# Performance work log

Hardware: AMD Instinct MI355X
Metric: run time of the kernel (lower is better)

The kernel has to match this reference:

```python
import math
import jax, jax.numpy as jnp
import numpy as np

N, E = 20000, 640000
S_DIM, Z_DIM, H, QK, VD = 64, 64, 4, 8, 8
EPS = 1e-8


def quat_rotate(v, q):
    # v: [..., 3], q: [..., 4] (w, x, y, z), broadcastable. Unit-quaternion rotation:
    # v' = v + 2*(w*(u x v) + u x (u x v))
    w = q[..., 0:1]
    u = q[..., 1:4]
    uv = jnp.cross(u, v)
    return v + 2.0 * (w * uv + jnp.cross(u, uv))


def setup_inputs() -> dict:
    key = jax.random.key(0)
    ks = jax.random.split(key, 16)
    s = jax.random.normal(ks[0], (N, S_DIM), dtype=jnp.float32)
    z = jax.random.normal(ks[1], (E, Z_DIM), dtype=jnp.float32)
    edge_index = jax.random.randint(ks[2], (2, E), 0, N)
    quaternion = jax.random.normal(ks[3], (N, 4), dtype=jnp.float32)
    quaternion = quaternion / jnp.linalg.norm(quaternion, axis=-1, keepdims=True)
    translation = jax.random.normal(ks[4], (N, 3), dtype=jnp.float32)
    sc_s = 1.0 / math.sqrt(S_DIM)
    sc_z = 1.0 / math.sqrt(Z_DIM)
    # weights stored [in, out] so y = x @ W (equivalent to torch x @ W.T)
    Wq_s = jax.random.normal(ks[5], (S_DIM, H * S_DIM), dtype=jnp.float32) * sc_s
    Wk_s = jax.random.normal(ks[6], (S_DIM, H * S_DIM), dtype=jnp.float32) * sc_s
    Wv_s = jax.random.normal(ks[7], (S_DIM, H * S_DIM), dtype=jnp.float32) * sc_s
    Wq_v = jax.random.normal(ks[8], (S_DIM, H * QK * 3), dtype=jnp.float32) * sc_s
    Wk_v = jax.random.normal(ks[9], (S_DIM, H * QK * 3), dtype=jnp.float32) * sc_s
    Wv_v = jax.random.normal(ks[10], (S_DIM, H * VD * 3), dtype=jnp.float32) * sc_s
    Wb = jax.random.normal(ks[11], (Z_DIM, H), dtype=jnp.float32) * sc_z
    bb = jnp.zeros((H,), dtype=jnp.float32)
    Wdz = jax.random.normal(ks[12], (Z_DIM, Z_DIM // 4), dtype=jnp.float32) * sc_z
    bdz = jnp.zeros((Z_DIM // 4,), dtype=jnp.float32)
    head_weights = jnp.full((H,), 0.541324854612918, dtype=jnp.float32)  # softplus^{-1}(1)
    concat_dim = Z_DIM // 4 + S_DIM + VD * 4
    Wout = jax.random.normal(ks[13], (H * concat_dim, S_DIM), dtype=jnp.float32) / math.sqrt(H * concat_dim)
    bout = jnp.zeros((S_DIM,), dtype=jnp.float32)
    return {
        's': s, 'z': z, 'edge_index': edge_index, 'quaternion': quaternion,
        'translation': translation, 'Wq_s': Wq_s, 'Wk_s': Wk_s, 'Wv_s': Wv_s,
        'Wq_v': Wq_v, 'Wk_v': Wk_v, 'Wv_v': Wv_v, 'Wb': Wb, 'bb': bb,
        'Wdz': Wdz, 'bdz': bdz, 'head_weights': head_weights,
        'Wout': Wout, 'bout': bout,
    }


def reference(s, z, edge_index, quaternion, translation,
              Wq_s, Wk_s, Wv_s, Wq_v, Wk_v, Wv_v,
              Wb, bb, Wdz, bdz, head_weights, Wout, bout):
    idx_i, idx_j = edge_index[0], edge_index[1]
    n = s.shape[0]
    h = head_weights.shape[0]
    qk = Wq_v.shape[1] // (3 * h)
    vd = Wv_v.shape[1] // (3 * h)

    q_scalar = (s @ Wq_s).reshape(n, h, -1)
    k_scalar = (s @ Wk_s).reshape(n, h, -1)
    v_scalar = (s @ Wv_s).reshape(n, h, -1)

    def to_points(x):
        # torch.split into 3 chunks then stack(dim=-1): [n, 3*c] -> [n, c, 3]
        c = x.shape[-1] // 3
        return jnp.swapaxes(x.reshape(n, 3, c), 1, 2)

    quat_b = quaternion[:, None, :]
    trans_b = translation[:, None, :]
    q_vec = (quat_rotate(to_points(s @ Wq_v), quat_b) + trans_b).reshape(n, h, qk, 3)
    k_vec = (quat_rotate(to_points(s @ Wk_v), quat_b) + trans_b).reshape(n, h, qk, 3)
    v_vec = (quat_rotate(to_points(s @ Wv_v), quat_b) + trans_b).reshape(n, h, vd, 3)

    b_bias = z @ Wb + bb  # [E, H]

    attn = jnp.sum(k_scalar[idx_i] * q_scalar[idx_j], axis=-1)  # [E, H]
    attn = attn * math.sqrt(1.0 / 3 * qk) + math.sqrt(1.0 / 3) * b_bias

    disp = q_vec[idx_i] - k_vec[idx_j]            # [E, H, qk, 3]
    vec_att = jnp.sum(disp * disp, axis=-1)       # [E, H, qk]
    hw = jax.nn.softplus(head_weights)[None, :, None]
    vec_att = jnp.sum(vec_att * hw, axis=-1) * math.sqrt(1.0 / (3 * (qk * 9.0 / 2))) * (-0.5)
    attn = attn + vec_att

    # segment softmax over destination node idx_i
    seg_max = jax.ops.segment_max(attn, idx_i, num_segments=n)
    ea = jnp.exp(attn - seg_max[idx_i])
    denom = jax.ops.segment_sum(ea, idx_i, num_segments=n)
    attn = ea / denom[idx_i]                      # [E, H]

    out_scalar = jax.ops.segment_sum(attn[:, :, None] * v_scalar[idx_i], idx_i, num_segments=n)
    out_scalar = out_scalar.reshape(n, -1)

    out_vec = jax.ops.segment_sum(attn[:, :, None, None] * v_vec[idx_i], idx_i, num_segments=n)
    out_vec = out_vec - translation[:, None, None, :]
    q_conj = jnp.concatenate([quaternion[:, :1], -quaternion[:, 1:]], axis=-1)
    out_vec = quat_rotate(out_vec, q_conj[:, None, None, :])   # [n, h, vd, 3]
    out_vec_norm = jnp.sqrt(jnp.sum(out_vec * out_vec, axis=-1) + EPS).reshape(n, -1)
    out_vec_flat = out_vec.reshape(n, -1, 3)

    pair_z = z @ Wdz + bdz                         # [E, z/4]
    out_pair = jax.ops.segment_sum(attn[:, :, None] * pair_z[:, None, :], idx_i, num_segments=n)
    out_pair = out_pair.reshape(n, -1)

    feats = jnp.concatenate([out_scalar,
                             out_vec_flat[..., 0], out_vec_flat[..., 1], out_vec_flat[..., 2],
                             out_vec_norm, out_pair], axis=-1)
    return feats @ Wout + bout
```

## Files before the change

### kernel.cpp

```cpp
#include <hip/hip_runtime.h>
#include <stdint.h>


#define C_SQRT83  1.6329931618554518f
#define C_SQRT13  0.5773502691896258f
#define C_VEC    -0.04811252243246881f

__device__ __forceinline__ unsigned short f2bf(float f){
  unsigned u = __float_as_uint(f);
  u += 0x7fffu + ((u >> 16) & 1u);
  return (unsigned short)(u >> 16);
}
__device__ __forceinline__ unsigned pack2(float a, float b){
  return (unsigned)f2bf(a) | ((unsigned)f2bf(b) << 16);
}
__device__ __forceinline__ float bflo(unsigned u){ return __uint_as_float(u << 16); }
__device__ __forceinline__ float bfhi(unsigned u){ return __uint_as_float(u & 0xffff0000u); }

__device__ __forceinline__ void quat_rot(float w, float ux, float uy, float uz,
                                         float vx, float vy, float vz,
                                         float& ox, float& oy, float& oz){
  float cx = uy*vz - uz*vy;
  float cy = uz*vx - ux*vz;
  float cz = ux*vy - uy*vx;
  float dx = uy*cz - uz*cy;
  float dy = uz*cx - ux*cz;
  float dz = ux*cy - uy*cx;
  ox = vx + 2.f*(w*cx + dx);
  oy = vy + 2.f*(w*cy + dy);
  oz = vz + 2.f*(w*cz + dz);
}


__global__ __launch_bounds__(256) void k_count(const int* __restrict__ ei,
                                               unsigned* __restrict__ counts,
                                               unsigned* __restrict__ rank, int ne){
  int e = blockIdx.x*256 + threadIdx.x;
  if (e >= ne) return;
  rank[e] = atomicAdd(&counts[ei[e]], 1u);
}

__global__ __launch_bounds__(256) void k_scan(const unsigned* __restrict__ counts,
                                              unsigned* __restrict__ row_off, int n){
  __shared__ unsigned part[256];
  int t = threadIdx.x;
  int chunk = (n + 255) >> 8;
  int s0 = t*chunk, s1 = min(s0 + chunk, n);
  unsigned sum = 0;
  for (int k = s0; k < s1; ++k) sum += counts[k];
  part[t] = sum; __syncthreads();
  for (int off = 1; off < 256; off <<= 1){
    unsigned v = (t >= off) ? part[t-off] : 0u;
    __syncthreads();
    part[t] += v;
    __syncthreads();
  }
  unsigned run = (t == 0) ? 0u : part[t-1];
  for (int k = s0; k < s1; ++k){
    row_off[k] = run; run += counts[k];
  }
  if (t == 255) row_off[n] = part[255];
}

__global__ __launch_bounds__(256) void k_fill(const int* __restrict__ ei,
                                              const unsigned* __restrict__ rank,
                                              const unsigned* __restrict__ roff,
                                              unsigned* __restrict__ si,
                                              unsigned* __restrict__ sj,
                                              unsigned* __restrict__ se, int ne){
  int e = blockIdx.x*256 + threadIdx.x;
  if (e >= ne) return;
  const int i = ei[e];
  const unsigned pos = roff[i] + rank[e];
  si[pos] = (unsigned)i;
  sj[pos] = (unsigned)ei[ne + e];
  se[pos] = (unsigned)e;
}


#define BN 32

__device__ __forceinline__ void pass256(const float* __restrict__ W,
                                        const float stT[64][40], int cg, int sl,
                                        float acc[8][4]){
  #pragma unroll
  for (int i=0;i<8;i++){ acc[i][0]=0.f; acc[i][1]=0.f; acc[i][2]=0.f; acc[i][3]=0.f; }
  #pragma unroll 4
  for (int k = 0; k < 64; ++k){
    const float4 w  = *(const float4*)(W + (size_t)k*256 + cg*4);
    const float4 n0 = *(const float4*)&stT[k][sl*8];
    const float4 n1 = *(const float4*)&stT[k][sl*8+4];
    acc[0][0]+=n0.x*w.x; acc[0][1]+=n0.x*w.y; acc[0][2]+=n0.x*w.z; acc[0][3]+=n0.x*w.w;
    acc[1][0]+=n0.y*w.x; acc[1][1]+=n0.y*w.y; acc[1][2]+=n0.y*w.z; acc[1][3]+=n0.y*w.w;
    acc[2][0]+=n0.z*w.x; acc[2][1]+=n0.z*w.y; acc[2][2]+=n0.z*w.z; acc[2][3]+=n0.z*w.w;
    acc[3][0]+=n0.w*w.x; acc[3][1]+=n0.w*w.y; acc[3][2]+=n0.w*w.z; acc[3][3]+=n0.w*w.w;
    acc[4][0]+=n1.x*w.x; acc[4][1]+=n1.x*w.y; acc[4][2]+=n1.x*w.z; acc[4][3]+=n1.x*w.w;
    acc[5][0]+=n1.y*w.x; acc[5][1]+=n1.y*w.y; acc[5][2]+=n1.y*w.z; acc[5][3]+=n1.y*w.w;
    acc[6][0]+=n1.z*w.x; acc[6][1]+=n1.z*w.y; acc[6][2]+=n1.z*w.z; acc[6][3]+=n1.z*w.w;
    acc[7][0]+=n1.w*w.x; acc[7][1]+=n1.w*w.y; acc[7][2]+=n1.w*w.z; acc[7][3]+=n1.w*w.w;
  }
}

__device__ __forceinline__ void pass96(const float* __restrict__ W,
                                       const float stT[64][40], int cgp, int slp,
                                       float acc[4][4]){
  #pragma unroll
  for (int i=0;i<4;i++){ acc[i][0]=0.f; acc[i][1]=0.f; acc[i][2]=0.f; acc[i][3]=0.f; }
  if (cgp >= 24) return;
  #pragma unroll 4
  for (int k = 0; k < 64; ++k){
    const float4 w = *(const float4*)(W + (size_t)k*96 + cgp*4);
    const float4 nv = *(const float4*)&stT[k][slp*4];
    acc[0][0]+=nv.x*w.x; acc[0][1]+=nv.x*w.y; acc[0][2]+=nv.x*w.z; acc[0][3]+=nv.x*w.w;
    acc[1][0]+=nv.y*w.x; acc[1][1]+=nv.y*w.y; acc[1][2]+=nv.y*w.z; acc[1][3]+=nv.y*w.w;
    acc[2][0]+=nv.z*w.x; acc[2][1]+=nv.z*w.y; acc[2][2]+=nv.z*w.z; acc[2][3]+=nv.z*w.w;
    acc[3][0]+=nv.w*w.x; acc[3][1]+=nv.w*w.y; acc[3][2]+=nv.w*w.z; acc[3][3]+=nv.w*w.w;
  }
}

__global__ __launch_bounds__(256) void k_proj(
    const float* __restrict__ s, const float* __restrict__ quat, const float* __restrict__ trans,
    const float* __restrict__ Wqs, const float* __restrict__ Wks, const float* __restrict__ Wvs,
    const float* __restrict__ Wqv, const float* __restrict__ Wkv, const float* __restrict__ Wvv,
    unsigned* __restrict__ qs, unsigned* __restrict__ ks, float* __restrict__ vs,
    unsigned* __restrict__ qv, unsigned* __restrict__ kv, float* __restrict__ vv, int n)
{
  __shared__ float stT[64][40];
  __shared__ float pt[BN][97];
  const int tid = threadIdx.x;
  const int node0 = blockIdx.x * BN;

  #pragma unroll
  for (int r = 0; r < 2; ++r){
    const int idx = tid + r*256;
    const int nd = idx >> 4, c4 = idx & 15;
    const int g = node0 + nd;
    float4 v = make_float4(0.f,0.f,0.f,0.f);
    if (g < n) v = *(const float4*)(s + (size_t)g*64 + c4*4);
    stT[c4*4+0][nd]=v.x; stT[c4*4+1][nd]=v.y; stT[c4*4+2][nd]=v.z; stT[c4*4+3][nd]=v.w;
  }
  __syncthreads();

  const int cg = tid & 63, sl = tid >> 6;
  const int cgp = tid & 31, slp = tid >> 5;
  float acc[8][4];

  pass256(Wqs, stT, cg, sl, acc);
  #pragma unroll
  for (int i=0;i<8;i++){
    const int g = node0 + sl*8 + i;
    if (g < n){
      uint2 u; u.x = pack2(acc[i][0],acc[i][1]); u.y = pack2(acc[i][2],acc[i][3]);
      *(uint2*)(qs + (size_t)g*128 + cg*2) = u;
    }
  }
  pass256(Wks, stT, cg, sl, acc);
  #pragma unroll
  for (int i=0;i<8;i++){
    const int g = node0 + sl*8 + i;
    if (g < n){
      uint2 u; u.x = pack2(acc[i][0],acc[i][1]); u.y = pack2(acc[i][2],acc[i][3]);
      *(uint2*)(ks + (size_t)g*128 + cg*2) = u;
    }
  }
  pass256(Wvs, stT, cg, sl, acc);
  #pragma unroll
  for (int i=0;i<8;i++){
    const int g = node0 + sl*8 + i;
    if (g < n){
      float4 f; f.x=acc[i][0]; f.y=acc[i][1]; f.z=acc[i][2]; f.w=acc[i][3];
      *(float4*)(vs + (size_t)g*256 + cg*4) = f;
    }
  }

  float pac[4][4];

  pass96(Wqv, stT, cgp, slp, pac);
  __syncthreads();
  if (cgp < 24){
    #pragma unroll
    for (int i=0;i<4;i++){
      #pragma unroll
      for (int c=0;c<4;c++) pt[slp*4+i][cgp*4+c] = pac[i][c];
    }
  }
  __syncthreads();
  #pragma unroll
  for (int r = 0; r < 2; ++r){
    const int t2 = tid + r*256;
    const int nd = t2 >> 4, pp = t2 & 15;
    const int g = node0 + nd;
    if (g < n){
      const float4 q4 = *(const float4*)(quat + (size_t)g*4);
      const float tx = trans[(size_t)g*3], ty = trans[(size_t)g*3+1], tz = trans[(size_t)g*3+2];
      float x0,y0,z0,x1,y1,z1;
      quat_rot(q4.x,q4.y,q4.z,q4.w, pt[nd][2*pp],   pt[nd][32+2*pp],   pt[nd][64+2*pp],   x0,y0,z0);
      quat_rot(q4.x,q4.y,q4.z,q4.w, pt[nd][2*pp+1], pt[nd][32+2*pp+1], pt[nd][64+2*pp+1], x1,y1,z1);
      x0+=tx; y0+=ty; z0+=tz; x1+=tx; y1+=ty; z1+=tz;
      unsigned* d = qv + (size_t)g*48 + pp*3;
      d[0] = pack2(x0,y0); d[1] = pack2(z0,x1); d[2] = pack2(y1,z1);
    }
  }

  pass96(Wkv, stT, cgp, slp, pac);
  __syncthreads();
  if (cgp < 24){
    #pragma unroll
    for (int i=0;i<4;i++){
      #pragma unroll
      for (int c=0;c<4;c++) pt[slp*4+i][cgp*4+c] = pac[i][c];
    }
  }
  __syncthreads();
  #pragma unroll
  for (int r = 0; r < 2; ++r){
    const int t2 = tid + r*256;
    const int nd = t2 >> 4, pp = t2 & 15;
    const int g = node0 + nd;
    if (g < n){
      const float4 q4 = *(const float4*)(quat + (size_t)g*4);
      const float tx = trans[(size_t)g*3], ty = trans[(size_t)g*3+1], tz = trans[(size_t)g*3+2];
      float x0,y0,z0,x1,y1,z1;
      quat_rot(q4.x,q4.y,q4.z,q4.w, pt[nd][2*pp],   pt[nd][32+2*pp],   pt[nd][64+2*pp],   x0,y0,z0);
      quat_rot(q4.x,q4.y,q4.z,q4.w, pt[nd][2*pp+1], pt[nd][32+2*pp+1], pt[nd][64+2*pp+1], x1,y1,z1);
      x0+=tx; y0+=ty; z0+=tz; x1+=tx; y1+=ty; z1+=tz;
      unsigned* d = kv + (size_t)g*48 + pp*3;
      d[0] = pack2(x0,y0); d[1] = pack2(z0,x1); d[2] = pack2(y1,z1);
    }
  }

  pass96(Wvv, stT, cgp, slp, pac);
  __syncthreads();
  if (cgp < 24){
    #pragma unroll
    for (int i=0;i<4;i++){
      #pragma unroll
      for (int c=0;c<4;c++) pt[slp*4+i][cgp*4+c] = pac[i][c];
    }
  }
  __syncthreads();
  #pragma unroll
  for (int r = 0; r < 12; ++r){
    const int idx = tid + r*256;
    const int nd = idx / 96, col = idx - nd*96;
    const int g = node0 + nd;
    if (g < n) vv[(size_t)g*96 + col] = pt[nd][col];
  }
}


__global__ __launch_bounds__(256) void k_edge(
    const float* __restrict__ z,
    const unsigned* __restrict__ si, const unsigned* __restrict__ sj, const unsigned* __restrict__ se,
    const float* __restrict__ Wb,  const float* __restrict__ bb,
    const float* __restrict__ Wdz, const float* __restrict__ bdz,
    const float* __restrict__ hwts,
    const unsigned* __restrict__ qs, const unsigned* __restrict__ ks,
    const unsigned* __restrict__ qv, const unsigned* __restrict__ kv,
    float* __restrict__ logits, unsigned* __restrict__ pz, int ne)
{
  const int p = blockIdx.x*256 + threadIdx.x;
  if (p >= ne) return;
  const unsigned i = si[p], j = sj[p], e = se[p];

  float b4[4];  b4[0]=b4[1]=b4[2]=b4[3]=0.f;
  float pacc[16];
  #pragma unroll
  for (int c=0;c<16;c++) pacc[c]=0.f;
  const float* zr = z + (size_t)e*64;
  #pragma unroll
  for (int k4 = 0; k4 < 16; ++k4){
    const float4 zv = *(const float4*)(zr + 4*k4);
    #pragma unroll
    for (int kk = 0; kk < 4; ++kk){
      const int k = 4*k4 + kk;
      const float zk = (kk==0)?zv.x:((kk==1)?zv.y:((kk==2)?zv.z:zv.w));
      const float4 wb = *(const float4*)(Wb + k*4);
      b4[0]+=zk*wb.x; b4[1]+=zk*wb.y; b4[2]+=zk*wb.z; b4[3]+=zk*wb.w;
      const float* wd = Wdz + k*16;
      const float4 w0=*(const float4*)(wd), w1=*(const float4*)(wd+4),
                   w2=*(const float4*)(wd+8), w3=*(const float4*)(wd+12);
      pacc[ 0]+=zk*w0.x; pacc[ 1]+=zk*w0.y; pacc[ 2]+=zk*w0.z; pacc[ 3]+=zk*w0.w;
      pacc[ 4]+=zk*w1.x; pacc[ 5]+=zk*w1.y; pacc[ 6]+=zk*w1.z; pacc[ 7]+=zk*w1.w;
      pacc[ 8]+=zk*w2.x; pacc[ 9]+=zk*w2.y; pacc[10]+=zk*w2.z; pacc[11]+=zk*w2.w;
      pacc[12]+=zk*w3.x; pacc[13]+=zk*w3.y; pacc[14]+=zk*w3.z; pacc[15]+=zk*w3.w;
    }
  }
  #pragma unroll
  for (int c=0;c<16;c++) pacc[c] += bdz[c];
  { uint4 u0, u1;
    u0.x=pack2(pacc[0],pacc[1]);   u0.y=pack2(pacc[2],pacc[3]);
    u0.z=pack2(pacc[4],pacc[5]);   u0.w=pack2(pacc[6],pacc[7]);
    u1.x=pack2(pacc[8],pacc[9]);   u1.y=pack2(pacc[10],pacc[11]);
    u1.z=pack2(pacc[12],pacc[13]); u1.w=pack2(pacc[14],pacc[15]);
    uint4* d = (uint4*)(pz + (size_t)p*8);
    d[0]=u0; d[1]=u1; }

  const uint4* kr = (const uint4*)(ks + (size_t)i*128);
  const uint4* qr = (const uint4*)(qs + (size_t)j*128);
  float sdot[4];
  #pragma unroll
  for (int h = 0; h < 4; ++h){
    float acc = 0.f;
    #pragma unroll
    for (int c = 0; c < 8; ++c){
      const uint4 a = kr[h*8+c];
      const uint4 b = qr[h*8+c];
      acc += bflo(a.x)*bflo(b.x) + bfhi(a.x)*bfhi(b.x);
      acc += bflo(a.y)*bflo(b.y) + bfhi(a.y)*bfhi(b.y);
      acc += bflo(a.z)*bflo(b.z) + bfhi(a.z)*bfhi(b.z);
      acc += bflo(a.w)*bflo(b.w) + bfhi(a.w)*bfhi(b.w);
    }
    sdot[h] = acc;
  }

  const uint4* qvr = (const uint4*)(qv + (size_t)i*48);
  const uint4* kvr = (const uint4*)(kv + (size_t)j*48);
  float vsum[4];
  #pragma unroll
  for (int h = 0; h < 4; ++h){
    float acc = 0.f;
    #pragma unroll
    for (int c = 0; c < 3; ++c){
      const uint4 a = qvr[h*3+c];
      const uint4 b = kvr[h*3+c];
      float d;
      d = bflo(a.x)-bflo(b.x); acc += d*d;  d = bfhi(a.x)-bfhi(b.x); acc += d*d;
      d = bflo(a.y)-bflo(b.y); acc += d*d;  d = bfhi(a.y)-bfhi(b.y); acc += d*d;
      d = bflo(a.z)-bflo(b.z); acc += d*d;  d = bfhi(a.z)-bfhi(b.z); acc += d*d;
      d = bflo(a.w)-bflo(b.w); acc += d*d;  d = bfhi(a.w)-bfhi(b.w); acc += d*d;
    }
    vsum[h] = acc;
  }

  float4 lg;
  {
    float l[4];
    #pragma unroll
    for (int h = 0; h < 4; ++h){
      const float hw = log1pf(__expf(hwts[h]));
      l[h] = C_SQRT83*sdot[h] + C_SQRT13*(b4[h] + bb[h]) + C_VEC*hw*vsum[h];
    }
    lg.x=l[0]; lg.y=l[1]; lg.z=l[2]; lg.w=l[3];
  }
  *(float4*)(logits + (size_t)p*4) = lg;
}


__global__ __launch_bounds__(256) void k_soft(
    const float* __restrict__ logits, const unsigned* __restrict__ pz,
    const unsigned* __restrict__ row_off, float* __restrict__ out_pair, int n)
{
  const int node = blockIdx.x*4 + (threadIdx.x >> 6);
  if (node >= n) return;
  const int lane = threadIdx.x & 63;
  const int beg = (int)row_off[node], end = (int)row_off[node+1];

  float m[4] = {-3.0e38f,-3.0e38f,-3.0e38f,-3.0e38f};
  for (int p = beg + lane; p < end; p += 64){
    const float4 l = *(const float4*)(logits + (size_t)p*4);
    m[0]=fmaxf(m[0],l.x); m[1]=fmaxf(m[1],l.y); m[2]=fmaxf(m[2],l.z); m[3]=fmaxf(m[3],l.w);
  }
  #pragma unroll
  for (int msk = 1; msk < 64; msk <<= 1){
    #pragma unroll
    for (int h=0;h<4;h++) m[h] = fmaxf(m[h], __shfl_xor(m[h], msk));
  }
  float S[4] = {0.f,0.f,0.f,0.f};
  for (int p = beg + lane; p < end; p += 64){
    const float4 l = *(const float4*)(logits + (size_t)p*4);
    S[0]+=__expf(l.x-m[0]); S[1]+=__expf(l.y-m[1]);
    S[2]+=__expf(l.z-m[2]); S[3]+=__expf(l.w-m[3]);
  }
  #pragma unroll
  for (int msk = 1; msk < 64; msk <<= 1){
    #pragma unroll
    for (int h=0;h<4;h++) S[h] += __shfl_xor(S[h], msk);
  }
  float inv[4];
  #pragma unroll
  for (int h=0;h<4;h++) inv[h] = (S[h] > 0.f) ? (1.f/S[h]) : 0.f;

  const int e4 = lane >> 4, c = lane & 15;
  float acc[4] = {0.f,0.f,0.f,0.f};
  for (int base = beg; base < end; base += 4){
    const int p = base + e4;
    if (p < end){
      const float4 l = *(const float4*)(logits + (size_t)p*4);
      const unsigned u = pz[(size_t)p*8 + (c>>1)];
      const float pzv = (c & 1) ? bfhi(u) : bflo(u);
      acc[0] += __expf(l.x-m[0]) * pzv;
      acc[1] += __expf(l.y-m[1]) * pzv;
      acc[2] += __expf(l.z-m[2]) * pzv;
      acc[3] += __expf(l.w-m[3]) * pzv;
    }
  }
  #pragma unroll
  for (int msk = 16; msk < 64; msk <<= 1){
    #pragma unroll
    for (int h=0;h<4;h++) acc[h] += __shfl_xor(acc[h], msk);
  }
  const int hOut = lane >> 4;
  out_pair[(size_t)node*64 + lane] = acc[hOut] * inv[hOut];
}


__global__ __launch_bounds__(256) void k_out(
    const float* __restrict__ vs, const float* __restrict__ vv,
    const float* __restrict__ out_pair, const unsigned* __restrict__ row_off,
    const float* __restrict__ quat, const float* __restrict__ trans,
    const float* __restrict__ Wout, const float* __restrict__ bout,
    float* __restrict__ out, int n)
{
  __shared__ float feats[32][448];
  __shared__ int degs[32];
  const int tid = threadIdx.x;
  const int node0 = blockIdx.x*32;

  if (tid < 32){
    const int g = node0 + tid;
    degs[tid] = (g < n) ? (int)(row_off[g+1] - row_off[g]) : 1;
  }
  __syncthreads();

  for (int x = tid; x < 32*256; x += 256){
    const int nd = x >> 8, c = x & 255;
    const int g = node0 + nd;
    feats[nd][c] = (g < n && degs[nd] > 0) ? vs[(size_t)g*256 + c] : 0.f;
  }
  for (int x = tid; x < 32*64; x += 256){
    const int nd = x >> 6, c = x & 63;
    const int g = node0 + nd;
    feats[nd][384 + c] = (g < n) ? out_pair[(size_t)g*64 + c] : 0.f;
  }
  for (int x = tid; x < 32*32; x += 256){
    const int nd = x >> 5, pt = x & 31;
    const int g = node0 + nd;
    float X=0.f, Y=0.f, Z=0.f;
    if (g < n){
      if (degs[nd] > 0){
        X = vv[(size_t)g*96 + pt];
        Y = vv[(size_t)g*96 + 32 + pt];
        Z = vv[(size_t)g*96 + 64 + pt];
      } else {
        const float4 q4 = *(const float4*)(quat + (size_t)g*4);
        const float tx = trans[(size_t)g*3], ty = trans[(size_t)g*3+1], tz = trans[(size_t)g*3+2];
        quat_rot(q4.x, -q4.y, -q4.z, -q4.w, -tx, -ty, -tz, X, Y, Z);
      }
    }
    feats[nd][256 + pt] = X;
    feats[nd][288 + pt] = Y;
    feats[nd][320 + pt] = Z;
    feats[nd][352 + pt] = sqrtf(X*X + Y*Y + Z*Z + 1e-8f);
  }
  __syncthreads();

  const int lane = tid & 63;
  const int wave = tid >> 6;
  float acc[8];
  #pragma unroll
  for (int q8=0;q8<8;q8++) acc[q8]=0.f;

  for (int k0 = 0; k0 < 448; k0 += 4){
    const float w0 = Wout[(size_t)(k0+0)*64 + lane];
    const float w1 = Wout[(size_t)(k0+1)*64 + lane];
    const float w2 = Wout[(size_t)(k0+2)*64 + lane];
    const float w3 = Wout[(size_t)(k0+3)*64 + lane];
    #pragma unroll
    for (int q8 = 0; q8 < 8; ++q8){
      const float4 f = *(const float4*)&feats[wave*8 + q8][k0];
      acc[q8] += f.x*w0 + f.y*w1 + f.z*w2 + f.w*w3;
    }
  }
  const float bo = bout[lane];
  #pragma unroll
  for (int q8 = 0; q8 < 8; ++q8){
    const int g = node0 + wave*8 + q8;
    if (g < n) out[(size_t)g*64 + lane] = acc[q8] + bo;
  }
}


extern "C" void kernel_launch(void* const* d_in, const int* in_sizes, int n_in,
                              void* d_out, int out_size, void* d_ws, size_t ws_size,
                              hipStream_t stream) {
  const float* s     = (const float*)d_in[0];
  const float* z     = (const float*)d_in[1];
  const int*   ei    = (const int*)  d_in[2];
  const float* quat  = (const float*)d_in[3];
  const float* trans = (const float*)d_in[4];
  const float* Wqs   = (const float*)d_in[5];
  const float* Wks   = (const float*)d_in[6];
  const float* Wvs   = (const float*)d_in[7];
  const float* Wqv   = (const float*)d_in[8];
  const float* Wkv   = (const float*)d_in[9];
  const float* Wvv   = (const float*)d_in[10];
  const float* Wb    = (const float*)d_in[11];
  const float* bb    = (const float*)d_in[12];
  const float* Wdz   = (const float*)d_in[13];
  const float* bdz   = (const float*)d_in[14];
  const float* hwts  = (const float*)d_in[15];
  const float* Wout  = (const float*)d_in[16];
  const float* bout  = (const float*)d_in[17];
  float* out = (float*)d_out;

  const int n  = in_sizes[0] / 64;
  const int ne = in_sizes[1] / 64;

  size_t off = 0;
  char* base = (char*)d_ws;
  auto take = [&](size_t bytes)->char* {
    char* p = base + off;
    off += (bytes + 255) & ~(size_t)255;
    return p;
  };
  unsigned* qs     = (unsigned*)take((size_t)n*512);
  unsigned* ks     = (unsigned*)take((size_t)n*512);
  unsigned* qvt    = (unsigned*)take((size_t)n*192);
  unsigned* kvt    = (unsigned*)take((size_t)n*192);
  float*    vs     = (float*)   take((size_t)n*1024);
  float*    vv     = (float*)   take((size_t)n*384);
  float*    logits = (float*)   take((size_t)ne*16);
  unsigned* pz     = (unsigned*)take((size_t)ne*32);
  unsigned* counts = (unsigned*)take((size_t)n*4);
  unsigned* roff   = (unsigned*)take((size_t)(n+1)*4);
  unsigned* rank   = (unsigned*)take((size_t)ne*4);
  unsigned* si     = (unsigned*)take((size_t)ne*4);
  unsigned* sj     = (unsigned*)take((size_t)ne*4);
  unsigned* se     = (unsigned*)take((size_t)ne*4);
  float*    opair  = (float*)   take((size_t)n*256);
  (void)ws_size; (void)n_in; (void)out_size;

  const int gbE = (ne + 255) / 256;

  hipMemsetAsync(counts, 0, (size_t)n*4, stream);
  k_count<<<gbE, 256, 0, stream>>>(ei, counts, rank, ne);
  k_scan <<<1,   256, 0, stream>>>(counts, roff, n);
  k_fill <<<gbE, 256, 0, stream>>>(ei, rank, roff, si, sj, se, ne);
  k_proj <<<(n + BN - 1)/BN, 256, 0, stream>>>(s, quat, trans, Wqs, Wks, Wvs, Wqv, Wkv, Wvv,
                                               qs, ks, vs, qvt, kvt, vv, n);
  k_edge <<<gbE, 256, 0, stream>>>(z, si, sj, se, Wb, bb, Wdz, bdz, hwts,
                                   qs, ks, qvt, kvt, logits, pz, ne);
  k_soft <<<(n + 3)/4, 256, 0, stream>>>(logits, pz, roff, opair, n);
  k_out  <<<(n + 31)/32, 256, 0, stream>>>(vs, vv, opair, roff, quat, trans,
                                           Wout, bout, out, n);
}
```

Before: 659.8 us.

## Split z projection into coalesced edge-order kernel, gather by edge id later

Moves the z @ Wb and z @ Wdz projections out of the sorted-order edge kernel into a separate kernel that reads z in original edge order, so the 64-float rows are read coalesced instead of gathered through the permutation. The edge kernel now gathers only a 16-byte bias row per edge, and the softmax kernel gathers the packed pair projection through se. This adds a kernel launch and an extra intermediate write and read of the bias, and it turns the pair reads in k_soft into indirect gathers.

```diff
diff --git a/kernel.cpp b/kernel.cpp
--- a/kernel.cpp
+++ b/kernel.cpp
@@ -249,24 +249,20 @@
 }
 
 
-__global__ __launch_bounds__(256) void k_edge(
+__global__ __launch_bounds__(256) void k_zp(
     const float* __restrict__ z,
-    const unsigned* __restrict__ si, const unsigned* __restrict__ sj, const unsigned* __restrict__ se,
     const float* __restrict__ Wb,  const float* __restrict__ bb,
     const float* __restrict__ Wdz, const float* __restrict__ bdz,
-    const float* __restrict__ hwts,
-    const unsigned* __restrict__ qs, const unsigned* __restrict__ ks,
-    const unsigned* __restrict__ qv, const unsigned* __restrict__ kv,
-    float* __restrict__ logits, unsigned* __restrict__ pz, int ne)
+    float* __restrict__ zb, unsigned* __restrict__ zpz, int ne)
 {
-  const int p = blockIdx.x*256 + threadIdx.x;
-  if (p >= ne) return;
-  const unsigned i = si[p], j = sj[p], e = se[p];
-
-  float b4[4];  b4[0]=b4[1]=b4[2]=b4[3]=0.f;
-  float pacc[16];
-  #pragma unroll
-  for (int c=0;c<16;c++) pacc[c]=0.f;
+  const int e = blockIdx.x*256 + threadIdx.x;
+  if (e >= ne) return;
+
+  float b4[4]; float pacc[16];
+  b4[0]=bb[0]; b4[1]=bb[1]; b4[2]=bb[2]; b4[3]=bb[3];
+  #pragma unroll
+  for (int c=0;c<16;c++) pacc[c] = bdz[c];
+
   const float* zr = z + (size_t)e*64;
   #pragma unroll
   for (int k4 = 0; k4 < 16; ++k4){
@@ -286,15 +282,30 @@
       pacc[12]+=zk*w3.x; pacc[13]+=zk*w3.y; pacc[14]+=zk*w3.z; pacc[15]+=zk*w3.w;
     }
   }
-  #pragma unroll
-  for (int c=0;c<16;c++) pacc[c] += bdz[c];
+  *(float4*)(zb + (size_t)e*4) = make_float4(b4[0],b4[1],b4[2],b4[3]);
   { uint4 u0, u1;
     u0.x=pack2(pacc[0],pacc[1]);   u0.y=pack2(pacc[2],pacc[3]);
     u0.z=pack2(pacc[4],pacc[5]);   u0.w=pack2(pacc[6],pacc[7]);
     u1.x=pack2(pacc[8],pacc[9]);   u1.y=pack2(pacc[10],pacc[11]);
     u1.z=pack2(pacc[12],pacc[13]); u1.w=pack2(pacc[14],pacc[15]);
-    uint4* d = (uint4*)(pz + (size_t)p*8);
+    uint4* d = (uint4*)(zpz + (size_t)e*8);
     d[0]=u0; d[1]=u1; }
+}
+
+
+__global__ __launch_bounds__(256) void k_edge(
+    const float* __restrict__ zb,
+    const unsigned* __restrict__ si, const unsigned* __restrict__ sj, const unsigned* __restrict__ se,
+    const float* __restrict__ hwts,
+    const unsigned* __restrict__ qs, const unsigned* __restrict__ ks,
+    const unsigned* __restrict__ qv, const unsigned* __restrict__ kv,
+    float* __restrict__ logits, int ne)
+{
+  const int p = blockIdx.x*256 + threadIdx.x;
+  if (p >= ne) return;
+  const unsigned i = si[p], j = sj[p], e = se[p];
+
+  const float4 b4 = *(const float4*)(zb + (size_t)e*4);
 
   const uint4* kr = (const uint4*)(ks + (size_t)i*128);
   const uint4* qr = (const uint4*)(qs + (size_t)j*128);
@@ -333,13 +344,14 @@
     vsum[h] = acc;
   }
 
+  const float bias[4] = {b4.x, b4.y, b4.z, b4.w};
   float4 lg;
   {
     float l[4];
     #pragma unroll
     for (int h = 0; h < 4; ++h){
       const float hw = log1pf(__expf(hwts[h]));
-      l[h] = C_SQRT83*sdot[h] + C_SQRT13*(b4[h] + bb[h]) + C_VEC*hw*vsum[h];
+      l[h] = C_SQRT83*sdot[h] + C_SQRT13*bias[h] + C_VEC*hw*vsum[h];
     }
     lg.x=l[0]; lg.y=l[1]; lg.z=l[2]; lg.w=l[3];
   }
@@ -348,7 +360,8 @@
 
 
 __global__ __launch_bounds__(256) void k_soft(
-    const float* __restrict__ logits, const unsigned* __restrict__ pz,
+    const float* __restrict__ logits, const unsigned* __restrict__ zpz,
+    const unsigned* __restrict__ se,
     const unsigned* __restrict__ row_off, float* __restrict__ out_pair, int n)
 {
   const int node = blockIdx.x*4 + (threadIdx.x >> 6);
@@ -387,7 +400,8 @@
     const int p = base + e4;
     if (p < end){
       const float4 l = *(const float4*)(logits + (size_t)p*4);
-      const unsigned u = pz[(size_t)p*8 + (c>>1)];
+      const unsigned e = se[p];
+      const unsigned u = zpz[(size_t)e*8 + (c>>1)];
       const float pzv = (c & 1) ? bfhi(u) : bflo(u);
       acc[0] += __expf(l.x-m[0]) * pzv;
       acc[1] += __expf(l.y-m[1]) * pzv;
@@ -521,7 +535,8 @@
   float*    vs     = (float*)   take((size_t)n*1024);
   float*    vv     = (float*)   take((size_t)n*384);
   float*    logits = (float*)   take((size_t)ne*16);
-  unsigned* pz     = (unsigned*)take((size_t)ne*32);
+  float*    zb     = (float*)   take((size_t)ne*16);
+  unsigned* zpz    = (unsigned*)take((size_t)ne*32);
   unsigned* counts = (unsigned*)take((size_t)n*4);
   unsigned* roff   = (unsigned*)take((size_t)(n+1)*4);
   unsigned* rank   = (unsigned*)take((size_t)ne*4);
@@ -539,9 +554,10 @@
   k_fill <<<gbE, 256, 0, stream>>>(ei, rank, roff, si, sj, se, ne);
   k_proj <<<(n + BN - 1)/BN, 256, 0, stream>>>(s, quat, trans, Wqs, Wks, Wvs, Wqv, Wkv, Wvv,
                                                qs, ks, vs, qvt, kvt, vv, n);
-  k_edge <<<gbE, 256, 0, stream>>>(z, si, sj, se, Wb, bb, Wdz, bdz, hwts,
-                                   qs, ks, qvt, kvt, logits, pz, ne);
-  k_soft <<<(n + 3)/4, 256, 0, stream>>>(logits, pz, roff, opair, n);
+  k_zp   <<<gbE, 256, 0, stream>>>(z, Wb, bb, Wdz, bdz, zb, zpz, ne);
+  k_edge <<<gbE, 256, 0, stream>>>(zb, si, sj, se, hwts,
+                                   qs, ks, qvt, kvt, logits, ne);
+  k_soft <<<(n + 3)/4, 256, 0, stream>>>(logits, zpz, se, roff, opair, n);
   k_out  <<<(n + 31)/32, 256, 0, stream>>>(vs, vv, opair, roff, quat, trans,
                                            Wout, bout, out, n);
 }
```

Result: slower. 710.6 us (+7.7%).
